# Performance work log

Measured on AMD Instinct MI355X. Metric: run time of the kernel, lower is better.

The kernel has to match this reference:

```python
import jax, jax.numpy as jnp
from jax import lax
import numpy as np

B, S, U, T = 128, 512, 1024, 48


def setup_inputs() -> dict:
    key = jax.random.key(0)
    ks = jax.random.split(key, 8)
    H = jax.random.normal(ks[0], (B, S, U), dtype=jnp.float32)
    tag = jax.random.randint(ks[1], (B, S), 0, T, dtype=jnp.int64 if jax.config.read('jax_enable_x64') else jnp.int32)
    s_len = jax.random.randint(ks[2], (B,), 1, S + 1, dtype=tag.dtype)
    w_mask = (jnp.arange(S)[None, :] < s_len[:, None]).astype(jnp.float32)
    # learned params (affine + CRF transitions), per param_init scales
    limit = float(np.sqrt(6.0 / (U + T)))  # xavier_uniform
    W = jax.random.uniform(ks[3], (U, T), minval=-limit, maxval=limit, dtype=jnp.float32)
    b = jnp.zeros((T,), dtype=jnp.float32)
    start_transitions = jax.random.uniform(ks[4], (T,), minval=-0.1, maxval=0.1, dtype=jnp.float32)
    end_transitions = jax.random.uniform(ks[5], (T,), minval=-0.1, maxval=0.1, dtype=jnp.float32)
    transitions = jax.random.uniform(ks[6], (T, T), minval=-0.1, maxval=0.1, dtype=jnp.float32)
    return {"H": H, "W": W, "b": b, "start_transitions": start_transitions,
            "end_transitions": end_transitions, "transitions": transitions,
            "tag": tag, "s_len": s_len, "w_mask": w_mask}


def _crf_log_likelihood(H, W, b, start_transitions, end_transitions, transitions, tag, s_len, w_mask):
    scores = jnp.einsum('bsu,ut->bst', H, W) + b  # (B,S,T) emissions
    # ---- numerator: score of the gold tag path ----
    emit_tag = jnp.take_along_axis(scores, tag[..., None], axis=2)[..., 0]  # (B,S)
    num = start_transitions[tag[:, 0]]
    num = num + jnp.sum(emit_tag * w_mask, axis=1)
    tr = transitions[tag[:, :-1], tag[:, 1:]]  # (B,S-1)
    num = num + jnp.sum(tr * w_mask[:, 1:], axis=1)
    last_tags = jnp.take_along_axis(tag, (s_len - 1)[:, None], axis=1)[:, 0]
    num = num + end_transitions[last_tags]
    # ---- partition: forward algorithm via scan over time ----
    log_prob0 = start_transitions[None, :] + scores[:, 0, :]  # (B,T)

    def step(log_prob, xs):
        emit_i, m_i = xs  # (B,T), (B,)
        # (B,T_prev,1) + (1,T_prev,T_next) + (B,1,T_next) -> lse over T_prev
        new = jax.nn.logsumexp(log_prob[:, :, None] + transitions[None, :, :] + emit_i[:, None, :], axis=1)
        log_prob = jnp.where(m_i[:, None] > 0, new, log_prob)
        return log_prob, None

    xs = (jnp.moveaxis(scores[:, 1:, :], 1, 0), w_mask[:, 1:].T)  # time-major
    log_prob, _ = lax.scan(step, log_prob0, xs)
    log_Z = jax.nn.logsumexp(log_prob + end_transitions[None, :], axis=1)  # (B,)
    return num - log_Z


def reference(H, W, b, start_transitions, end_transitions, transitions, tag, s_len, w_mask):
    return _crf_log_likelihood(H, W, b, start_transitions, end_transitions, transitions, tag, s_len, w_mask)
```

## Files before the change

kernel.cpp:

```cpp
#include <hip/hip_runtime.h>
#include <math.h>

#define B_  128
#define S_  512
#define U_  1024
#define T_  48

typedef short  bf16x8 __attribute__((ext_vector_type(8)));
typedef float  f32x4  __attribute__((ext_vector_type(4)));

__device__ __forceinline__ unsigned pack_bf16(float lo, float hi) {
    const unsigned a = __float_as_uint(lo) + 0x8000u;
    const unsigned b = __float_as_uint(hi) + 0x8000u;
    return __builtin_amdgcn_perm(b, a, 0x07060302u);
}

__global__ __launch_bounds__(256) void prep_w(
    const float* __restrict__ W, unsigned short* __restrict__ Wt)
{
    const int n = blockIdx.x;
#pragma unroll
    for (int i = 0; i < 4; ++i) {
        const int k = threadIdx.x + 256 * i;
        const unsigned u = __float_as_uint(W[(size_t)k * T_ + n]) + 0x8000u;
        Wt[(size_t)n * U_ + k] = (unsigned short)(u >> 16);
    }
}

#define KC     64
#define HS_LD  72
#define WS_LD  72

__global__ __launch_bounds__(256) void gemm_scores_mfma(
    const float* __restrict__ H, const unsigned short* __restrict__ Wt,
    const float* __restrict__ bias, const int* __restrict__ s_len,
    float* __restrict__ scores, float* __restrict__ emit)
{
    __shared__ unsigned short Hs[128 * HS_LD];
    __shared__ unsigned short Ws[T_ * WS_LD];

    const int blk = blockIdx.x;
    const int b   = blk >> 2;
    const int s0  = (blk & 3) * 128;
    if (s0 >= s_len[b]) return;

    const int tid  = threadIdx.x;
    const int wave = tid >> 6;
    const int lane = tid & 63;
    const int m16  = lane & 15;
    const int q    = lane >> 4;
    const int grp  = tid >> 4;
    const int l16  = tid & 15;

    const size_t row0 = (size_t)b * S_ + s0;
    const float* Hg = H + row0 * U_;

    f32x4 acc[2][3];
#pragma unroll
    for (int mt = 0; mt < 2; ++mt)
#pragma unroll
        for (int nt = 0; nt < 3; ++nt) acc[mt][nt] = (f32x4){0.f, 0.f, 0.f, 0.f};

    for (int kc = 0; kc < U_ / KC; ++kc) {
        const int k0 = kc * KC;

#pragma unroll
        for (int p = 0; p < 8; ++p) {
            const int row = p * 16 + grp;
            const float4 h = *reinterpret_cast<const float4*>(
                Hg + (size_t)row * U_ + k0 + l16 * 4);
            const unsigned p01 = pack_bf16(h.x, h.y);
            const unsigned p23 = pack_bf16(h.z, h.w);
            *reinterpret_cast<uint2*>(&Hs[row * HS_LD + l16 * 4]) =
                make_uint2(p01, p23);
        }
#pragma unroll
        for (int i = 0; i < 2; ++i) {
            const int idx = tid + 256 * i;
            if (idx < 384) {
                const int n = idx >> 3, seg = idx & 7;
                const uint4 w = *reinterpret_cast<const uint4*>(
                    Wt + (size_t)n * U_ + k0 + seg * 8);
                *reinterpret_cast<uint4*>(&Ws[n * WS_LD + seg * 8]) = w;
            }
        }
        __syncthreads();

        bf16x8 afr[2][2], bfr[3][2];
#pragma unroll
        for (int mt = 0; mt < 2; ++mt)
#pragma unroll
            for (int ks = 0; ks < 2; ++ks)
                afr[mt][ks] = *reinterpret_cast<const bf16x8*>(
                    &Hs[(wave * 32 + mt * 16 + m16) * HS_LD + ks * 32 + q * 8]);
#pragma unroll
        for (int nt = 0; nt < 3; ++nt)
#pragma unroll
            for (int ks = 0; ks < 2; ++ks)
                bfr[nt][ks] = *reinterpret_cast<const bf16x8*>(
                    &Ws[(nt * 16 + m16) * WS_LD + ks * 32 + q * 8]);
#pragma unroll
        for (int ks = 0; ks < 2; ++ks)
#pragma unroll
            for (int mt = 0; mt < 2; ++mt)
#pragma unroll
                for (int nt = 0; nt < 3; ++nt)
                    acc[mt][nt] = __builtin_amdgcn_mfma_f32_16x16x32_bf16(
                        afr[mt][ks], bfr[nt][ks], acc[mt][nt], 0, 0, 0);
        __syncthreads();
    }

#pragma unroll
    for (int mt = 0; mt < 2; ++mt) {
#pragma unroll
        for (int nt = 0; nt < 3; ++nt) {
            const int col = nt * 16 + m16;
            const float bv = bias[col];
#pragma unroll
            for (int i = 0; i < 4; ++i) {
                const size_t r = row0 + wave * 32 + mt * 16 + q * 4 + i;
                const float v = acc[mt][nt][i] + bv;
                scores[r * T_ + col] = v;
                emit[r * T_ + col]   = __expf(v);
            }
        }
    }
}

__device__ __forceinline__ float rfl(float x) {
    return __int_as_float(__builtin_amdgcn_readfirstlane(__float_as_int(x)));
}

__global__ __launch_bounds__(64) void crf_forward(
    const float* __restrict__ scores, const float* __restrict__ emit,
    const float* __restrict__ start_tr, const float* __restrict__ end_tr,
    const float* __restrict__ trans, const int* __restrict__ tag,
    const int* __restrict__ s_len, float* __restrict__ out)
{
    __shared__ float E[T_ * T_];
    __shared__ float Tr[T_ * T_];
    __shared__ __align__(16) float wb[2][64];

    const int b    = blockIdx.x;
    const int lane = threadIdx.x;

    for (int i = lane; i < T_ * T_; i += 64) {
        const float t = trans[i];
        Tr[i] = t;
        E[i]  = __expf(t);
    }
    __syncthreads();

    const int len = s_len[b];
    const float* sc = scores + (size_t)b * S_ * T_;
    const float* em = emit   + (size_t)b * S_ * T_;
    const int*   tg = tag + (size_t)b * S_;

    float nsum = 0.f;
    for (int s = lane; s < len; s += 64) {
        const int t = tg[s];
        nsum += sc[s * T_ + t];
        if (s >= 1) nsum += Tr[tg[s - 1] * T_ + t];
    }
#pragma unroll
    for (int off = 32; off >= 1; off >>= 1)
        nsum += __shfl_xor(nsum, off);

    const int col = (lane < T_) ? lane : 0;
    float e[T_];
#pragma unroll
    for (int j = 0; j < T_; ++j) e[j] = E[j * T_ + col];

    const float lp0 = (lane < T_) ? (start_tr[lane] + sc[lane]) : -1e30f;
    const float m0  = rfl(lp0);
    float v = __expf(lp0 - m0);
    float C = m0;
    float invr = 1.0f, lr = 0.0f;

#define CRF_STEP(EM, BUF)                                                   \
    {                                                                       \
        wb[BUF][lane] = v;                                                  \
        __builtin_amdgcn_wave_barrier();                                    \
        const float4* a4 = reinterpret_cast<const float4*>(wb[BUF]);        \
        float d0 = 0.f, d1 = 0.f, d2 = 0.f, d3 = 0.f;                       \
        float d4 = 0.f, d5 = 0.f, d6 = 0.f, d7 = 0.f;                       \
        _Pragma("unroll")                                                   \
        for (int j4 = 0; j4 < T_ / 8; ++j4) {                               \
            const float4 pa = a4[2 * j4];                                   \
            const float4 pb = a4[2 * j4 + 1];                               \
            d0 = fmaf(pa.x, e[8 * j4 + 0], d0);                             \
            d1 = fmaf(pa.y, e[8 * j4 + 1], d1);                             \
            d2 = fmaf(pa.z, e[8 * j4 + 2], d2);                             \
            d3 = fmaf(pa.w, e[8 * j4 + 3], d3);                             \
            d4 = fmaf(pb.x, e[8 * j4 + 4], d4);                             \
            d5 = fmaf(pb.y, e[8 * j4 + 5], d5);                             \
            d6 = fmaf(pb.z, e[8 * j4 + 6], d6);                             \
            d7 = fmaf(pb.w, e[8 * j4 + 7], d7);                             \
        }                                                                   \
        __builtin_amdgcn_wave_barrier();                                    \
        const float scl = (EM) * invr;         \
        const float dt  = ((d0 + d4) + (d1 + d5)) + ((d2 + d6) + (d3 + d7));\
        v = dt * scl;                                                       \
        C += lr;                                                            \
        const float r = rfl(v);              \
        invr = __builtin_amdgcn_rcpf(r);                                    \
        lr   = __logf(r);                                                   \
    }

    constexpr int PF = 8;
    int s = 1;
    while (s + PF <= len) {
        float emv[PF];
#pragma unroll
        for (int i = 0; i < PF; ++i) emv[i] = em[(s + i) * T_ + col];
#pragma unroll
        for (int i = 0; i < PF; ++i) CRF_STEP(emv[i], ((s + i) & 1));
        s += PF;
    }
    if (s < len) {
        const int rem = len - s;
        float emv[PF];
#pragma unroll
        for (int i = 0; i < PF; ++i)
            if (i < rem) emv[i] = em[(s + i) * T_ + col];
#pragma unroll
        for (int i = 0; i < PF; ++i)
            if (i < rem) CRF_STEP(emv[i], ((s + i) & 1));
    }
#undef CRF_STEP

    float z = (lane < T_) ? v * __expf(end_tr[lane]) : 0.f;
#pragma unroll
    for (int off = 32; off >= 1; off >>= 1)
        z += __shfl_xor(z, off);
    const float logZ = C + __logf(z);

    if (lane == 0) {
        const float num = nsum + start_tr[tg[0]] + end_tr[tg[len - 1]];
        out[b] = num - logZ;
    }
}

extern "C" void kernel_launch(void* const* d_in, const int* in_sizes, int n_in,
                              void* d_out, int out_size, void* d_ws, size_t ws_size,
                              hipStream_t stream) {
    const float* H        = (const float*)d_in[0];
    const float* W        = (const float*)d_in[1];
    const float* bias     = (const float*)d_in[2];
    const float* start_tr = (const float*)d_in[3];
    const float* end_tr   = (const float*)d_in[4];
    const float* trans    = (const float*)d_in[5];
    const int*   tag      = (const int*)d_in[6];
    const int*   s_len    = (const int*)d_in[7];

    const size_t NSC = (size_t)B_ * S_ * T_;
    float*          scores = (float*)d_ws;
    float*          emit   = scores + NSC;
    unsigned short* Wt     = (unsigned short*)(emit + NSC);

    hipLaunchKernelGGL(prep_w, dim3(T_), dim3(256), 0, stream, W, Wt);
    hipLaunchKernelGGL(gemm_scores_mfma, dim3((B_ * S_) / 128), dim3(256), 0, stream,
                       H, Wt, bias, s_len, scores, emit);
    hipLaunchKernelGGL(crf_forward, dim3(B_), dim3(64), 0, stream,
                       scores, emit, start_tr, end_tr, trans, tag, s_len,
                       (float*)d_out);
}
```

Baseline: 495.9 us.

## Parallelize CRF forward scan via chunked transfer-matrix products with MFMA

```diff
diff --git a/kernel.cpp b/kernel.cpp
--- a/kernel.cpp
+++ b/kernel.cpp
@@ -5,10 +5,16 @@
 #define S_  512
 #define U_  1024
 #define T_  48
+#define CHK 8
+#define NCH 64
+#define PLD 72
 
 typedef short  bf16x8 __attribute__((ext_vector_type(8)));
 typedef float  f32x4  __attribute__((ext_vector_type(4)));
 
+__device__ __forceinline__ float rfl(float x) {
+    return __int_as_float(__builtin_amdgcn_readfirstlane(__float_as_int(x)));
+}
 __device__ __forceinline__ unsigned pack_bf16(float lo, float hi) {
     const unsigned a = __float_as_uint(lo) + 0x8000u;
     const unsigned b = __float_as_uint(hi) + 0x8000u;
@@ -34,7 +40,7 @@
 __global__ __launch_bounds__(256) void gemm_scores_mfma(
     const float* __restrict__ H, const unsigned short* __restrict__ Wt,
     const float* __restrict__ bias, const int* __restrict__ s_len,
-    float* __restrict__ scores, float* __restrict__ emit)
+    float* __restrict__ scores)
 {
     __shared__ unsigned short Hs[128 * HS_LD];
     __shared__ unsigned short Ws[T_ * WS_LD];
@@ -63,7 +69,6 @@
 
     for (int kc = 0; kc < U_ / KC; ++kc) {
         const int k0 = kc * KC;
-
 #pragma unroll
         for (int p = 0; p < 8; ++p) {
             const int row = p * 16 + grp;
@@ -111,7 +116,7 @@
     }
 
 #pragma unroll
-    for (int mt = 0; mt < 2; ++mt) {
+    for (int mt = 0; mt < 2; ++mt)
 #pragma unroll
         for (int nt = 0; nt < 3; ++nt) {
             const int col = nt * 16 + m16;
@@ -119,20 +124,151 @@
 #pragma unroll
             for (int i = 0; i < 4; ++i) {
                 const size_t r = row0 + wave * 32 + mt * 16 + q * 4 + i;
-                const float v = acc[mt][nt][i] + bv;
-                scores[r * T_ + col] = v;
-                emit[r * T_ + col]   = __expf(v);
+                scores[r * T_ + col] = acc[mt][nt][i] + bv;
             }
         }
-    }
-}
-
-__device__ __forceinline__ float rfl(float x) {
-    return __int_as_float(__builtin_amdgcn_readfirstlane(__float_as_int(x)));
+}
+
+__global__ __launch_bounds__(256) void build_ops(
+    const float* __restrict__ scores, const float* __restrict__ trans,
+    const int* __restrict__ s_len,
+    unsigned short* __restrict__ Ptg, float* __restrict__ logS)
+{
+    __shared__ float Eld[T_ * T_];
+    __shared__ __align__(16) unsigned short Pb[4 * 48 * PLD];
+
+    const int tid  = threadIdx.x;
+    const int wid  = tid >> 6;
+    const int lane = tid & 63;
+    const int m16  = lane & 15;
+    const int q    = lane >> 4;
+
+    for (int i = tid; i < T_ * T_; i += 256)
+        Eld[i] = __expf(trans[i]);
+    __syncthreads();
+
+    const int widx = blockIdx.x * 4 + wid;
+    const int b    = widx >> 6;
+    const int c    = widx & (NCH - 1);
+    const int len  = s_len[b];
+    const int s0   = 1 + c * CHK;
+    if (s0 + CHK > len) return;
+
+    unsigned short* Ps = &Pb[wid * 48 * PLD];
+
+    bf16x8 afr[3][2];
+#pragma unroll
+    for (int mt = 0; mt < 3; ++mt)
+#pragma unroll
+        for (int kt = 0; kt < 2; ++kt) {
+            union { bf16x8 v; unsigned short s[8]; } u;
+#pragma unroll
+            for (int j = 0; j < 8; ++j) {
+                const int k = kt * 32 + q * 8 + j;
+                const int m = mt * 16 + m16;
+                const float ev = (k < T_) ? Eld[k * T_ + m] : 0.f;
+                u.s[j] = (unsigned short)((__float_as_uint(ev) + 0x8000u) >> 16);
+            }
+            afr[mt][kt] = u.v;
+        }
+
+    {
+        uint4* p4 = reinterpret_cast<uint4*>(Ps);
+        const uint4 z = make_uint4(0u, 0u, 0u, 0u);
+        for (int i = lane; i < 48 * PLD / 8; i += 64) p4[i] = z;
+        __builtin_amdgcn_wave_barrier();
+        if (lane < T_) Ps[lane * PLD + lane] = 0x3F80;
+        __builtin_amdgcn_wave_barrier();
+    }
+
+    const float* sb = scores + ((size_t)b * S_ + s0) * T_;
+    float logacc = 0.f;
+
+    float4 emld[3];
+#pragma unroll
+    for (int mt = 0; mt < 3; ++mt)
+        emld[mt] = reinterpret_cast<const float4*>(sb)[mt * 4 + q];
+
+    for (int i = 0; i < CHK; ++i) {
+        float4 em[3];
+#pragma unroll
+        for (int mt = 0; mt < 3; ++mt) {
+            em[mt].x = __expf(emld[mt].x); em[mt].y = __expf(emld[mt].y);
+            em[mt].z = __expf(emld[mt].z); em[mt].w = __expf(emld[mt].w);
+        }
+        if (i + 1 < CHK) {
+            const float* sn = sb + (i + 1) * T_;
+#pragma unroll
+            for (int mt = 0; mt < 3; ++mt)
+                emld[mt] = reinterpret_cast<const float4*>(sn)[mt * 4 + q];
+        }
+
+        bf16x8 bfr[2][3];
+#pragma unroll
+        for (int kt = 0; kt < 2; ++kt)
+#pragma unroll
+            for (int nt = 0; nt < 3; ++nt)
+                bfr[kt][nt] = *reinterpret_cast<const bf16x8*>(
+                    &Ps[(nt * 16 + m16) * PLD + kt * 32 + q * 8]);
+
+        f32x4 acc[3][3];
+#pragma unroll
+        for (int mt = 0; mt < 3; ++mt)
+#pragma unroll
+            for (int nt = 0; nt < 3; ++nt) acc[mt][nt] = (f32x4){0.f,0.f,0.f,0.f};
+#pragma unroll
+        for (int kt = 0; kt < 2; ++kt)
+#pragma unroll
+            for (int mt = 0; mt < 3; ++mt)
+#pragma unroll
+                for (int nt = 0; nt < 3; ++nt)
+                    acc[mt][nt] = __builtin_amdgcn_mfma_f32_16x16x32_bf16(
+                        afr[mt][kt], bfr[kt][nt], acc[mt][nt], 0, 0, 0);
+
+        const float r    = rfl(acc[0][0][0] * em[0].x);
+        const float rinv = __builtin_amdgcn_rcpf(r);
+        logacc += __logf(r);
+        __builtin_amdgcn_wave_barrier();
+#pragma unroll
+        for (int mt = 0; mt < 3; ++mt) {
+            const float sx = em[mt].x * rinv, sy = em[mt].y * rinv;
+            const float sz = em[mt].z * rinv, sw = em[mt].w * rinv;
+#pragma unroll
+            for (int nt = 0; nt < 3; ++nt) {
+                const unsigned lo = pack_bf16(acc[mt][nt][0] * sx,
+                                              acc[mt][nt][1] * sy);
+                const unsigned hi = pack_bf16(acc[mt][nt][2] * sz,
+                                              acc[mt][nt][3] * sw);
+                *reinterpret_cast<uint2*>(
+                    &Ps[(nt * 16 + m16) * PLD + mt * 16 + q * 4]) =
+                    make_uint2(lo, hi);
+            }
+        }
+        __builtin_amdgcn_wave_barrier();
+    }
+
+    if (lane < T_) {
+        unsigned outp[24];
+#pragma unroll
+        for (int j2 = 0; j2 < 24; ++j2) {
+            const unsigned a  = Ps[(2 * j2)     * PLD + lane];
+            const unsigned b2 = Ps[(2 * j2 + 1) * PLD + lane];
+            outp[j2] = a | (b2 << 16);
+        }
+        unsigned short* dst =
+            Ptg + (((size_t)b * NCH + c) * 48 + lane) * 48;
+        uint4* d4 = reinterpret_cast<uint4*>(dst);
+#pragma unroll
+        for (int t4 = 0; t4 < 6; ++t4)
+            d4[t4] = make_uint4(outp[4*t4], outp[4*t4+1],
+                                outp[4*t4+2], outp[4*t4+3]);
+    }
+    if (lane == 0) logS[(size_t)b * NCH + c] = logacc;
 }
 
 __global__ __launch_bounds__(64) void crf_forward(
-    const float* __restrict__ scores, const float* __restrict__ emit,
+    const float* __restrict__ scores, const unsigned short* __restrict__ Ptg,
+    const float* __restrict__ logS,
     const float* __restrict__ start_tr, const float* __restrict__ end_tr,
     const float* __restrict__ trans, const int* __restrict__ tag,
     const int* __restrict__ s_len, float* __restrict__ out)
@@ -153,7 +289,6 @@
 
     const int len = s_len[b];
     const float* sc = scores + (size_t)b * S_ * T_;
-    const float* em = emit   + (size_t)b * S_ * T_;
     const int*   tg = tag + (size_t)b * S_;
 
     float nsum = 0.f;
@@ -167,65 +302,120 @@
         nsum += __shfl_xor(nsum, off);
 
     const int col = (lane < T_) ? lane : 0;
-    float e[T_];
-#pragma unroll
-    for (int j = 0; j < T_; ++j) e[j] = E[j * T_ + col];
 
     const float lp0 = (lane < T_) ? (start_tr[lane] + sc[lane]) : -1e30f;
     const float m0  = rfl(lp0);
     float v = __expf(lp0 - m0);
     float C = m0;
     float invr = 1.0f, lr = 0.0f;
+    int par = 0;
+
+    const int F = (len - 1) / CHK;
+    const unsigned short* Pb_ = Ptg + (size_t)b * NCH * 48 * 48;
+    const float* Lb = logS + (size_t)b * NCH;
+
+    uint4 cur[6], nxt[6];
+    float ls_cur = 0.f, ls_nxt = 0.f;
+    if (F > 0) {
+        const uint4* p = reinterpret_cast<const uint4*>(Pb_ + (size_t)col * 48);
+#pragma unroll
+        for (int i = 0; i < 6; ++i) cur[i] = p[i];
+        ls_cur = Lb[0];
+    }
+    for (int cc = 0; cc < F; ++cc) {
+        if (cc + 1 < F) {
+            const uint4* p = reinterpret_cast<const uint4*>(
+                Pb_ + (size_t)(cc + 1) * 2304 + (size_t)col * 48);
+#pragma unroll
+            for (int i = 0; i < 6; ++i) nxt[i] = p[i];
+            ls_nxt = Lb[cc + 1];
+        }
+        float pr[48];
+#pragma unroll
+        for (int i = 0; i < 6; ++i) {
+            const uint4 u = cur[i];
+            pr[8*i+0] = __uint_as_float(u.x << 16);
+            pr[8*i+1] = __uint_as_float(u.x & 0xFFFF0000u);
+            pr[8*i+2] = __uint_as_float(u.y << 16);
+            pr[8*i+3] = __uint_as_float(u.y & 0xFFFF0000u);
+            pr[8*i+4] = __uint_as_float(u.z << 16);
+            pr[8*i+5] = __uint_as_float(u.z & 0xFFFF0000u);
+            pr[8*i+6] = __uint_as_float(u.w << 16);
+            pr[8*i+7] = __uint_as_float(u.w & 0xFFFF0000u);
+        }
+        wb[par & 1][lane] = v;
+        __builtin_amdgcn_wave_barrier();
+        const float4* a4 = reinterpret_cast<const float4*>(wb[par & 1]);
+        float d0=0.f,d1=0.f,d2=0.f,d3=0.f,d4=0.f,d5=0.f,d6=0.f,d7=0.f;
+#pragma unroll
+        for (int j4 = 0; j4 < 6; ++j4) {
+            const float4 pa = a4[2 * j4];
+            const float4 pb = a4[2 * j4 + 1];
+            d0 = fmaf(pa.x, pr[8*j4+0], d0);
+            d1 = fmaf(pa.y, pr[8*j4+1], d1);
+            d2 = fmaf(pa.z, pr[8*j4+2], d2);
+            d3 = fmaf(pa.w, pr[8*j4+3], d3);
+            d4 = fmaf(pb.x, pr[8*j4+4], d4);
+            d5 = fmaf(pb.y, pr[8*j4+5], d5);
+            d6 = fmaf(pb.z, pr[8*j4+6], d6);
+            d7 = fmaf(pb.w, pr[8*j4+7], d7);
+        }
+        __builtin_amdgcn_wave_barrier();
+        const float dt = ((d0 + d4) + (d1 + d5)) + ((d2 + d6) + (d3 + d7));
+        v = dt * invr;
+        C += lr + ls_cur;
+        const float r = rfl(v);
+        invr = __builtin_amdgcn_rcpf(r);
+        lr   = __logf(r);
+        par ^= 1;
+#pragma unroll
+        for (int i = 0; i < 6; ++i) cur[i] = nxt[i];
+        ls_cur = ls_nxt;
+    }
+
+    float e[T_];
+#pragma unroll
+    for (int j = 0; j < T_; ++j) e[j] = E[j * T_ + col];
 
 #define CRF_STEP(EM, BUF)                                                   \
     {                                                                       \
         wb[BUF][lane] = v;                                                  \
         __builtin_amdgcn_wave_barrier();                                    \
-        const float4* a4 = reinterpret_cast<const float4*>(wb[BUF]);        \
-        float d0 = 0.f, d1 = 0.f, d2 = 0.f, d3 = 0.f;                       \
-        float d4 = 0.f, d5 = 0.f, d6 = 0.f, d7 = 0.f;                       \
+        const float4* a4t = reinterpret_cast<const float4*>(wb[BUF]);       \
+        float t0=0.f,t1=0.f,t2=0.f,t3=0.f,t4=0.f,t5=0.f,t6=0.f,t7=0.f;      \
         _Pragma("unroll")                                                   \
-        for (int j4 = 0; j4 < T_ / 8; ++j4) {                               \
-            const float4 pa = a4[2 * j4];                                   \
-            const float4 pb = a4[2 * j4 + 1];                               \
-            d0 = fmaf(pa.x, e[8 * j4 + 0], d0);                             \
-            d1 = fmaf(pa.y, e[8 * j4 + 1], d1);                             \
-            d2 = fmaf(pa.z, e[8 * j4 + 2], d2);                             \
-            d3 = fmaf(pa.w, e[8 * j4 + 3], d3);                             \
-            d4 = fmaf(pb.x, e[8 * j4 + 4], d4);                             \
-            d5 = fmaf(pb.y, e[8 * j4 + 5], d5);                             \
-            d6 = fmaf(pb.z, e[8 * j4 + 6], d6);                             \
-            d7 = fmaf(pb.w, e[8 * j4 + 7], d7);                             \
+        for (int j4 = 0; j4 < 6; ++j4) {                                    \
+            const float4 pa = a4t[2 * j4];                                  \
+            const float4 pb = a4t[2 * j4 + 1];                              \
+            t0 = fmaf(pa.x, e[8*j4+0], t0);                                 \
+            t1 = fmaf(pa.y, e[8*j4+1], t1);                                 \
+            t2 = fmaf(pa.z, e[8*j4+2], t2);                                 \
+            t3 = fmaf(pa.w, e[8*j4+3], t3);                                 \
+            t4 = fmaf(pb.x, e[8*j4+4], t4);                                 \
+            t5 = fmaf(pb.y, e[8*j4+5], t5);                                 \
+            t6 = fmaf(pb.z, e[8*j4+6], t6);                                 \
+            t7 = fmaf(pb.w, e[8*j4+7], t7);                                 \
         }                                                                   \
         __builtin_amdgcn_wave_barrier();                                    \
-        const float scl = (EM) * invr;         \
-        const float dt  = ((d0 + d4) + (d1 + d5)) + ((d2 + d6) + (d3 + d7));\
-        v = dt * scl;                                                       \
+        const float scl = (EM) * invr;                                      \
+        const float dtt = ((t0 + t4) + (t1 + t5)) + ((t2 + t6) + (t3 + t7));\
+        v = dtt * scl;                                                      \
         C += lr;                                                            \
-        const float r = rfl(v);              \
-        invr = __builtin_amdgcn_rcpf(r);                                    \
-        lr   = __logf(r);                                                   \
-    }
-
-    constexpr int PF = 8;
-    int s = 1;
-    while (s + PF <= len) {
-        float emv[PF];
-#pragma unroll
-        for (int i = 0; i < PF; ++i) emv[i] = em[(s + i) * T_ + col];
-#pragma unroll
-        for (int i = 0; i < PF; ++i) CRF_STEP(emv[i], ((s + i) & 1));
-        s += PF;
-    }
-    if (s < len) {
-        const int rem = len - s;
-        float emv[PF];
-#pragma unroll
-        for (int i = 0; i < PF; ++i)
-            if (i < rem) emv[i] = em[(s + i) * T_ + col];
-#pragma unroll
-        for (int i = 0; i < PF; ++i)
-            if (i < rem) CRF_STEP(emv[i], ((s + i) & 1));
+        const float r2 = rfl(v);                                            \
+        invr = __builtin_amdgcn_rcpf(r2);                                   \
+        lr   = __logf(r2);                                                  \
+    }
+
+    const int st = 1 + F * CHK;
+    if (st < len) {
+        const int rem = len - st;
+        float emv[CHK - 1];
+#pragma unroll
+        for (int i = 0; i < CHK - 1; ++i)
+            if (i < rem) emv[i] = __expf(sc[(st + i) * T_ + col]);
+#pragma unroll
+        for (int i = 0; i < CHK - 1; ++i)
+            if (i < rem) { CRF_STEP(emv[i], (par & 1)); par ^= 1; }
     }
 #undef CRF_STEP
 
@@ -255,13 +445,16 @@
 
     const size_t NSC = (size_t)B_ * S_ * T_;
     float*          scores = (float*)d_ws;
-    float*          emit   = scores + NSC;
-    unsigned short* Wt     = (unsigned short*)(emit + NSC);
+    float*          logS   = scores + NSC;
+    unsigned short* Wt     = (unsigned short*)(logS + B_ * NCH);
+    unsigned short* Ptg    = Wt + (size_t)T_ * U_;
 
     hipLaunchKernelGGL(prep_w, dim3(T_), dim3(256), 0, stream, W, Wt);
-    hipLaunchKernelGGL(gemm_scores_mfma, dim3((B_ * S_) / 128), dim3(256), 0, stream,
-                       H, Wt, bias, s_len, scores, emit);
+    hipLaunchKernelGGL(gemm_scores_mfma, dim3((B_ * S_) / 128), dim3(256), 0,
+                       stream, H, Wt, bias, s_len, scores);
+    hipLaunchKernelGGL(build_ops, dim3(B_ * NCH / 4), dim3(256), 0, stream,
+                       scores, trans, s_len, Ptg, logS);
     hipLaunchKernelGGL(crf_forward, dim3(B_), dim3(64), 0, stream,
-                       scores, emit, start_tr, end_tr, trans, tag, s_len,
+                       scores, Ptg, logS, start_tr, end_tr, trans, tag, s_len,
                        (float*)d_out);
 }
```

Result: faster. 456.7 us (-7.9%).
